# Performance work log

Hardware: AMD Instinct MI355X
Metric: run time of the kernel (lower is better)

Reference implementation:

```python
import jax, jax.numpy as jnp
import numpy as np
import math

EPS = 1e-5
GROUPS = 32

def group_norm(x, gamma, beta, groups=GROUPS, eps=EPS):
    B, C, H, W = x.shape
    xr = x.reshape(B, groups, C // groups, H, W)
    m = xr.mean(axis=(2, 3, 4), keepdims=True)
    v = xr.var(axis=(2, 3, 4), keepdims=True)
    xr = (xr - m) * jax.lax.rsqrt(v + eps)
    x = xr.reshape(B, C, H, W)
    return x * gamma[None, :, None, None] + beta[None, :, None, None]

def swish(x):
    return x * jax.nn.sigmoid(x)

def conv2d(x, w, b=None, padding='SAME'):
    # x: NCHW, w: OIHW
    y = jax.lax.conv_general_dilated(x, w, window_strides=(1, 1), padding=padding,
                                     dimension_numbers=('NCHW', 'OIHW', 'NCHW'))
    if b is not None:
        y = y + b[None, :, None, None]
    return y

def setup_inputs() -> dict:
    key = jax.random.key(0)
    ks = jax.random.split(key, 24)
    B, C, H, W = 16, 256, 32, 32
    NE = 256  # noise_level_emb_dim
    s = 0.02
    inp = {
        'x': jax.random.normal(ks[0], (B, C, H, W), jnp.float32),
        'time_emb': jax.random.normal(ks[1], (B, NE), jnp.float32),
        'c': jax.random.normal(ks[2], (B, C, H, W), jnp.float32),
        # block1: GroupNorm + Swish + Conv3x3(dim -> dim_out)
        'gn1_g': jnp.ones((C,), jnp.float32),
        'gn1_b': jnp.zeros((C,), jnp.float32),
        'conv1_w': jax.random.normal(ks[3], (C, C, 3, 3), jnp.float32) * s,
        'conv1_b': jnp.zeros((C,), jnp.float32),
        # FeatureWiseAffine linear (use_affine_level=False): Linear(NE -> dim_out)
        'noise_w': jax.random.normal(ks[4], (C, NE), jnp.float32) * s,
        'noise_b': jnp.zeros((C,), jnp.float32),
        # block2: GroupNorm + Swish + Conv3x3(dim_out -> dim_out)
        'gn2_g': jnp.ones((C,), jnp.float32),
        'gn2_b': jnp.zeros((C,), jnp.float32),
        'conv2_w': jax.random.normal(ks[5], (C, C, 3, 3), jnp.float32) * s,
        'conv2_b': jnp.zeros((C,), jnp.float32),
        # c_func: Conv1x1(dim_out -> dim_out)
        'cfunc_w': jax.random.normal(ks[6], (C, C, 1, 1), jnp.float32) * s,
        'cfunc_b': jnp.zeros((C,), jnp.float32),
        # attention: GroupNorm, qkv Conv1x1 (no bias), out Conv1x1
        'attn_gn_g': jnp.ones((C,), jnp.float32),
        'attn_gn_b': jnp.zeros((C,), jnp.float32),
        'qkv_w': jax.random.normal(ks[7], (3 * C, C, 1, 1), jnp.float32) * s,
        'out_w': jax.random.normal(ks[8], (C, C, 1, 1), jnp.float32) * s,
        'out_b': jnp.zeros((C,), jnp.float32),
    }
    return inp

def reference(x, time_emb, c,
              gn1_g, gn1_b, conv1_w, conv1_b,
              noise_w, noise_b,
              gn2_g, gn2_b, conv2_w, conv2_b,
              cfunc_w, cfunc_b,
              attn_gn_g, attn_gn_b, qkv_w, out_w, out_b):
    B, C, H, W = x.shape
    # ---- ResnetBlock ----
    h = conv2d(swish(group_norm(x, gn1_g, gn1_b)), conv1_w, conv1_b)
    # FeatureWiseAffine (additive): h + Linear(time_emb) broadcast over HxW
    h = h + (time_emb @ noise_w.T + noise_b)[:, :, None, None]
    h = conv2d(swish(group_norm(h, gn2_g, gn2_b)), conv2_w, conv2_b)
    h = conv2d(c, cfunc_w, cfunc_b) + h
    h = h + x  # res_conv is Identity since dim == dim_out
    # ---- SelfAttention (n_head=1) ----
    n = group_norm(h, attn_gn_g, attn_gn_b)
    qkv = conv2d(n, qkv_w)                       # [B, 3C, H, W]
    q, k, v = jnp.split(qkv.reshape(B, 3 * C, H * W), 3, axis=1)  # each [B, C, HW]
    scores = jnp.einsum('bcs,bct->bst', q, k) / math.sqrt(C)      # [B, HW, HW]
    attn = jax.nn.softmax(scores, axis=-1)
    o = jnp.einsum('bst,bct->bcs', attn, v).reshape(B, C, H, W)
    o = conv2d(o, out_w, out_b)
    return o + h
```

## Files before the change

kernel.cpp:

```cpp
#include <hip/hip_runtime.h>
#include <hip/hip_bf16.h>
#include <math.h>

typedef __hip_bfloat16 bf16;
typedef short short8 __attribute__((ext_vector_type(8)));
typedef float floatx4 __attribute__((ext_vector_type(4)));

#define NB 16
#define NC 256
#define NHW 1024
#define NNE 256
#define NP (NB*NC*NHW)

__device__ __forceinline__ unsigned short f2bu(float f){
  bf16 h = (bf16)f; return *(unsigned short*)&h;
}

__device__ __forceinline__ void gload_lds16(const short* g, short* l){
  __builtin_amdgcn_global_load_lds(
      (const __attribute__((address_space(1))) void*)g,
      (__attribute__((address_space(3))) void*)l, 16, 0, 0);
}

template<bool SWISH>
__global__ void gn_t_kernel(const float* __restrict__ src, const float* __restrict__ gamma,
                            const float* __restrict__ beta, short* __restrict__ xp){
  int b = blockIdx.x >> 5, g = blockIdx.x & 31;
  const int GSZ = 8*NHW;
  size_t base = ((size_t)b*NC + g*8)*NHW;
  int tid = threadIdx.x;
  float s = 0.f, ss = 0.f;
  for (int i = tid; i < GSZ; i += 256){
    float v = src[base+i];
    s += v; ss += v*v;
  }
  __shared__ float rs[256], rq[256];
  rs[tid] = s; rq[tid] = ss;
  __syncthreads();
  for (int off=128; off>0; off>>=1){
    if (tid < off){ rs[tid]+=rs[tid+off]; rq[tid]+=rq[tid+off]; }
    __syncthreads();
  }
  float mean = rs[0] * (1.f/GSZ);
  float var  = rq[0] * (1.f/GSZ) - mean*mean;
  float inv  = rsqrtf(var + 1e-5f);
  float gm[8], bt[8];
  #pragma unroll
  for (int j=0;j<8;j++){ gm[j] = gamma[g*8+j]*inv; bt[j] = beta[g*8+j]; }
  short* dst = xp + (((size_t)b*8 + (g>>2))*NHW)*32 + (g&3)*8;
  for (int px = tid; px < NHW; px += 256){
    short8 pk;
    #pragma unroll
    for (int j=0;j<8;j++){
      float v = (src[base + j*NHW + px] - mean)*gm[j] + bt[j];
      if (SWISH) v = v / (1.f + __expf(-v));
      pk[j] = (short)f2bu(v);
    }
    *(short8*)(dst + (size_t)px*32) = pk;
  }
}

template<bool SWISH>
__global__ void gn_post_kernel(const float* __restrict__ src, const float* __restrict__ st,
                               const float* __restrict__ gamma, const float* __restrict__ beta,
                               short* __restrict__ xp){
  int b = blockIdx.x >> 5, g = blockIdx.x & 31;
  size_t base = ((size_t)b*NC + g*8)*NHW;
  int tid = threadIdx.x;
  float s  = st[(b*32+g)*2+0];
  float ss = st[(b*32+g)*2+1];
  float mean = s * (1.f/8192.f);
  float var  = ss * (1.f/8192.f) - mean*mean;
  float inv  = rsqrtf(var + 1e-5f);
  float gm[8], bt[8];
  #pragma unroll
  for (int j=0;j<8;j++){ gm[j] = gamma[g*8+j]*inv; bt[j] = beta[g*8+j]; }
  short* dst = xp + (((size_t)b*8 + (g>>2))*NHW)*32 + (g&3)*8;
  for (int px = tid; px < NHW; px += 256){
    short8 pk;
    #pragma unroll
    for (int j=0;j<8;j++){
      float v = (src[base + j*NHW + px] - mean)*gm[j] + bt[j];
      if (SWISH) v = v / (1.f + __expf(-v));
      pk[j] = (short)f2bu(v);
    }
    *(short8*)(dst + (size_t)px*32) = pk;
  }
}

__global__ void wprep3_kernel(const float* __restrict__ w1, const float* __restrict__ w2,
                              short* __restrict__ wp1, short* __restrict__ wp2,
                              float* __restrict__ st){
  int co = blockIdx.x & 255;
  const float* w = (blockIdx.x < 256) ? w1 : w2;
  short* wp = (blockIdx.x < 256) ? wp1 : wp2;
  int tid = threadIdx.x;
  if (blockIdx.x == 0){
    for (int i=tid;i<4096;i+=256) st[i] = 0.f;
  }
  __shared__ float tmp[2304];
  for (int i=tid;i<2304;i+=256) tmp[i] = w[(size_t)co*2304 + i];
  __syncthreads();
  for (int j=tid;j<2304;j+=256){
    int tap = j>>8, ci = j&255;
    wp[(((size_t)tap*8 + (ci>>5))*NC + co)*32 + (ci&31)] = (short)f2bu(tmp[ci*9 + tap]);
  }
}

__global__ void wprep1_kernel(const float* __restrict__ wq, const float* __restrict__ wc,
                              const float* __restrict__ wo,
                              short* __restrict__ wqp, short* __restrict__ wcp,
                              short* __restrict__ wop){
  int blk = blockIdx.x, tid = threadIdx.x;
  if (blk < 768){
    float v = wq[(size_t)blk*256 + tid];
    wqp[(((size_t)(tid>>5))*768 + blk)*32 + (tid&31)] = (short)f2bu(v);
  } else if (blk < 1024){
    int co = blk - 768;
    float v = wc[(size_t)co*256 + tid];
    wcp[(((size_t)(tid>>5))*256 + co)*32 + (tid&31)] = (short)f2bu(v);
  } else {
    int co = blk - 1024;
    float v = wo[(size_t)co*256 + tid];
    wop[(((size_t)(tid>>5))*256 + co)*32 + (tid&31)] = (short)f2bu(v);
  }
}

__global__ void cvtc_kernel(const float* __restrict__ c_in, short* __restrict__ cp){
  int pxc = blockIdx.x, cc = blockIdx.y, b = blockIdx.z, tid = threadIdx.x;
  __shared__ float ld[32][257];
  size_t gbase = ((size_t)b*NC + cc*32)*NHW + pxc*256;
  for (int j=0;j<32;j++) ld[j][tid] = c_in[gbase + (size_t)j*NHW + tid];
  __syncthreads();
  short* dst = cp + (((size_t)b*8 + cc)*NHW + pxc*256)*32;
  for (int it=0;it<4;it++){
    int pxl = it*64 + (tid>>2), ckl = tid&3;
    short8 pk;
    #pragma unroll
    for (int e=0;e<8;e++) pk[e] = (short)f2bu(ld[ckl*8+e][pxl]);
    *(short8*)(dst + (size_t)pxl*32 + ckl*8) = pk;
  }
}

__global__ void noise_kernel(const float* __restrict__ emb, const float* __restrict__ w,
                             const float* __restrict__ bias, float* __restrict__ na){
  int b = blockIdx.x, c = threadIdx.x;
  __shared__ float e[NNE];
  e[c] = emb[b*NNE + c];
  __syncthreads();
  float acc = bias[c];
  for (int k=0;k<NNE;k++) acc += e[k]*w[c*NNE+k];
  na[b*NC + c] = acc;
}

__global__ __launch_bounds__(256,2)
void conv3_mfma_kernel(const short* __restrict__ xp, const short* __restrict__ wp,
                       const float* __restrict__ bias, const float* __restrict__ bias_bc,
                       const float* __restrict__ addf, float* __restrict__ out,
                       float* __restrict__ st, const short* __restrict__ zpad){
  const int b = blockIdx.z, bx = blockIdx.x, by = blockIdx.y;
  const int tid = threadIdx.x, wave = tid>>6, lane = tid&63;
  const int quad = lane>>4, lm = lane&15;
  const int co0 = by*64;
  const int px0 = bx*128, yb = bx*4;

  __shared__ short Sb0[12288], Sb1[12288], Sb2[12288];

  const int rowt = tid>>3;
  const int g2   = (tid&7) ^ ((tid>>3)&7);
  const int kq2  = g2 & 3;
  const int ccs2 = g2 >> 2;
  const size_t b8 = (size_t)b*8*NHW*32;

  auto STAGE = [&](int j, short* S){
    const int tap = j>>2, ccp = j&3;
    const int dyp = (tap*11)>>5;
    const int dx  = tap - dyp*3 - 1;
    const int dy  = dyp - 1;
    const short* wsrc = wp + (size_t)(tap*8 + ccp*2 + ccs2)*8192 + (co0 + rowt)*32 + kq2*8;
    #pragma unroll
    for (int i=0;i<2;i++)
      gload_lds16(wsrc + i*(32*32), S + tid*8 + i*2048);
    const short* xstep = xp + b8 + (size_t)(ccp*2 + ccs2)*(NHW*32);
    const int xx = rowt + dx;
    const bool xok = (unsigned)xx < 32u;
    #pragma unroll
    for (int i=0;i<4;i++){
      const int y = yb + i + dy;
      const short* src = (xok && (unsigned)y < 32u)
                       ? (xstep + (y*32 + xx)*32 + kq2*8)
                       : (zpad + kq2*8);
      gload_lds16(src, S + 4096 + tid*8 + i*2048);
    }
  };

  floatx4 acc[4][2];
  #pragma unroll
  for (int mt=0;mt<4;mt++)
    #pragma unroll
    for (int nt=0;nt<2;nt++) acc[mt][nt] = (floatx4){0.f,0.f,0.f,0.f};

  const int sl = lm & 7;
  auto STEP = [&](int j, short* S){
    asm volatile("s_waitcnt vmcnt(12)" ::: "memory");
    __builtin_amdgcn_s_barrier();
    __builtin_amdgcn_sched_barrier(0);
    short8 Af[2][4], Bf[2][2];
    #pragma unroll
    for (int ka=0;ka<2;ka++){
      const int slot = ((ka*4 + quad) ^ sl) << 3;
      #pragma unroll
      for (int mt=0;mt<4;mt++)
        Af[ka][mt] = *(const short8*)(S + (mt*16+lm)*64 + slot);
      #pragma unroll
      for (int nt=0;nt<2;nt++)
        Bf[ka][nt] = *(const short8*)(S + 4096 + (wave*32 + nt*16 + lm)*64 + slot);
    }
    asm volatile("s_waitcnt lgkmcnt(0)" ::: "memory");
    __builtin_amdgcn_sched_barrier(0);
    __builtin_amdgcn_s_barrier();
    int jn = j + 3; if (jn > 35) jn = 35;
    STAGE(jn, S);
    __builtin_amdgcn_s_setprio(1);
    #pragma unroll
    for (int ka=0;ka<2;ka++)
      #pragma unroll
      for (int mt=0;mt<4;mt++)
        #pragma unroll
        for (int nt=0;nt<2;nt++)
          acc[mt][nt] = __builtin_amdgcn_mfma_f32_16x16x32_bf16(Af[ka][mt], Bf[ka][nt], acc[mt][nt], 0,0,0);
    __builtin_amdgcn_s_setprio(0);
  };

  STAGE(0, Sb0); STAGE(1, Sb1); STAGE(2, Sb2);
  for (int jt=0; jt<36; jt+=3){
    STEP(jt+0, Sb0);
    STEP(jt+1, Sb1);
    STEP(jt+2, Sb2);
  }

  float gs[4], gq[4];
  #pragma unroll
  for (int mt=0;mt<4;mt++){ gs[mt]=0.f; gq[mt]=0.f; }
  #pragma unroll
  for (int mt=0;mt<4;mt++){
    #pragma unroll
    for (int r=0;r<4;r++){
      int co = co0 + mt*16 + quad*4 + r;
      float bb = bias[co] + (bias_bc ? bias_bc[b*NC + co] : 0.f);
      size_t ob = ((size_t)b*NC + co)*NHW + px0 + wave*32;
      #pragma unroll
      for (int nt=0;nt<2;nt++){
        size_t oi = ob + nt*16 + lm;
        float v = acc[mt][nt][r] + bb;
        if (addf) v += addf[oi];
        out[oi] = v;
        gs[mt] += v; gq[mt] += v*v;
      }
    }
  }
  #pragma unroll
  for (int mt=0;mt<4;mt++){
    float s = gs[mt], q = gq[mt];
    #pragma unroll
    for (int o=1;o<32;o<<=1){ s += __shfl_xor(s, o, 64); q += __shfl_xor(q, o, 64); }
    if ((lane&31) == 0){
      int g = (co0>>3) + mt*2 + (quad>>1);
      atomicAdd(&st[(b*32+g)*2+0], s);
      atomicAdd(&st[(b*32+g)*2+1], q);
    }
  }
}

__global__ __launch_bounds__(256)
void gemm_cfunc_kernel(const short* __restrict__ cp, const short* __restrict__ wcp,
                       const float* __restrict__ bias, const float* __restrict__ xres,
                       float* __restrict__ out){
  const int b = blockIdx.z;
  const int tid = threadIdx.x, wave = tid>>6, lane = tid&63;
  const int quad = lane>>4, lm = lane&15;
  const int M0 = blockIdx.y*128 + (wave>>1)*64;
  const int N0 = blockIdx.x*128 + (wave&1)*64;
  floatx4 acc[4][4];
  #pragma unroll
  for (int mt=0;mt<4;mt++)
    #pragma unroll
    for (int nt=0;nt<4;nt++) acc[mt][nt] = (floatx4){0.f,0.f,0.f,0.f};
  #pragma unroll
  for (int kk=0;kk<8;kk++){
    short8 af[4], bfr[4];
    #pragma unroll
    for (int mt=0;mt<4;mt++)
      af[mt] = *(const short8*)(wcp + ((size_t)kk*256 + M0 + mt*16 + lm)*32 + quad*8);
    #pragma unroll
    for (int nt=0;nt<4;nt++)
      bfr[nt] = *(const short8*)(cp + (((size_t)b*8 + kk)*NHW + N0 + nt*16 + lm)*32 + quad*8);
    #pragma unroll
    for (int mt=0;mt<4;mt++)
      #pragma unroll
      for (int nt=0;nt<4;nt++)
        acc[mt][nt] = __builtin_amdgcn_mfma_f32_16x16x32_bf16(af[mt], bfr[nt], acc[mt][nt], 0,0,0);
  }
  #pragma unroll
  for (int mt=0;mt<4;mt++){
    #pragma unroll
    for (int r=0;r<4;r++){
      int co = M0 + mt*16 + quad*4 + r;
      float bb = bias[co];
      size_t ob = ((size_t)b*NC + co)*NHW + N0;
      #pragma unroll
      for (int nt=0;nt<4;nt++){
        size_t oi = ob + nt*16 + lm;
        out[oi] = acc[mt][nt][r] + bb + xres[oi];
      }
    }
  }
}

__global__ __launch_bounds__(256)
void gemm_qkv_kernel(const short* __restrict__ ntp, const short* __restrict__ wqp,
                     short* __restrict__ qp, short* __restrict__ kp, short* __restrict__ vp){
  const int b = blockIdx.z;
  const int tid = threadIdx.x, wave = tid>>6, lane = tid&63;
  const int quad = lane>>4, lm = lane&15;
  const int M0 = blockIdx.y*128 + (wave>>1)*64;
  const int N0 = blockIdx.x*128 + (wave&1)*64;
  floatx4 acc[4][4];
  #pragma unroll
  for (int mt=0;mt<4;mt++)
    #pragma unroll
    for (int nt=0;nt<4;nt++) acc[mt][nt] = (floatx4){0.f,0.f,0.f,0.f};
  #pragma unroll
  for (int kk=0;kk<8;kk++){
    short8 af[4], bfr[4];
    #pragma unroll
    for (int mt=0;mt<4;mt++)
      af[mt] = *(const short8*)(wqp + ((size_t)kk*768 + M0 + mt*16 + lm)*32 + quad*8);
    #pragma unroll
    for (int nt=0;nt<4;nt++)
      bfr[nt] = *(const short8*)(ntp + (((size_t)b*8 + kk)*NHW + N0 + nt*16 + lm)*32 + quad*8);
    #pragma unroll
    for (int mt=0;mt<4;mt++)
      #pragma unroll
      for (int nt=0;nt<4;nt++)
        acc[mt][nt] = __builtin_amdgcn_mfma_f32_16x16x32_bf16(af[mt], bfr[nt], acc[mt][nt], 0,0,0);
  }
  #pragma unroll
  for (int mt=0;mt<4;mt++){
    int co_base = M0 + mt*16 + quad*4;
    int sec = co_base >> 8;
    int c = co_base & 255;
    #pragma unroll
    for (int nt=0;nt<4;nt++){
      int s = N0 + nt*16 + lm;
      if (sec < 2){
        unsigned short t0 = f2bu(acc[mt][nt][0]), t1 = f2bu(acc[mt][nt][1]);
        unsigned short t2 = f2bu(acc[mt][nt][2]), t3 = f2bu(acc[mt][nt][3]);
        uint2 w2; w2.x = ((unsigned)t1<<16)|t0; w2.y = ((unsigned)t3<<16)|t2;
        short* dst = (sec==0) ? qp : kp;
        *(uint2*)(dst + (((size_t)b*8 + (c>>5))*NHW + s)*32 + (c&31)) = w2;
      } else {
        #pragma unroll
        for (int r=0;r<4;r++)
          vp[(((size_t)b*32 + (s>>5))*NC + c + r)*32 + (s&31)] = (short)f2bu(acc[mt][nt][r]);
      }
    }
  }
}

__global__ __launch_bounds__(1024)
void attn_mfma_kernel(const short* __restrict__ qp, const short* __restrict__ kp,
                      const short* __restrict__ vp, short* __restrict__ op){
  const int bx = blockIdx.x;
  const int b = bx & 15;
  const int s0 = (bx >> 4) * 64;
  const int tid = threadIdx.x, wave = tid>>6, lane = tid&63;
  const int quad = lane>>4, lm = lane&15;

  __shared__ short P[64*1024];
  __shared__ float red[64][16];
  __shared__ float fred[64];

  floatx4 sc[4][4];
  #pragma unroll
  for (int rt=0;rt<4;rt++)
    #pragma unroll
    for (int ti=0;ti<4;ti++) sc[rt][ti] = (floatx4){0.f,0.f,0.f,0.f};

  const int colb = wave*64;
  #pragma unroll
  for (int h=0;h<8;h++){
    const size_t hb = ((size_t)b*8 + h)*NHW;
    short8 aq[4], kf[4];
    #pragma unroll
    for (int rt=0;rt<4;rt++)
      aq[rt] = *(const short8*)(qp + (hb + s0 + rt*16 + lm)*32 + quad*8);
    #pragma unroll
    for (int ti=0;ti<4;ti++)
      kf[ti] = *(const short8*)(kp + (hb + colb + ti*16 + lm)*32 + quad*8);
    #pragma unroll
    for (int rt=0;rt<4;rt++)
      #pragma unroll
      for (int ti=0;ti<4;ti++)
        sc[rt][ti] = __builtin_amdgcn_mfma_f32_16x16x32_bf16(aq[rt], kf[ti], sc[rt][ti], 0,0,0);
  }

  const float scale = 0.0625f;
  float mx[4][4];
  #pragma unroll
  for (int rt=0;rt<4;rt++)
    #pragma unroll
    for (int r=0;r<4;r++) mx[rt][r] = -1e30f;
  #pragma unroll
  for (int rt=0;rt<4;rt++)
    #pragma unroll
    for (int ti=0;ti<4;ti++)
      #pragma unroll
      for (int r=0;r<4;r++){
        float v = sc[rt][ti][r]*scale;
        sc[rt][ti][r] = v;
        mx[rt][r] = fmaxf(mx[rt][r], v);
      }
  #pragma unroll
  for (int o=1;o<16;o<<=1)
    #pragma unroll
    for (int rt=0;rt<4;rt++)
      #pragma unroll
      for (int r=0;r<4;r++) mx[rt][r] = fmaxf(mx[rt][r], __shfl_xor(mx[rt][r], o, 64));
  if (lm==0){
    #pragma unroll
    for (int rt=0;rt<4;rt++)
      #pragma unroll
      for (int r=0;r<4;r++) red[rt*16 + quad*4 + r][wave] = mx[rt][r];
  }
  __syncthreads();
  {
    float v = red[tid>>4][tid&15];
    #pragma unroll
    for (int o=1;o<16;o<<=1) v = fmaxf(v, __shfl_xor(v, o, 64));
    if ((tid&15)==0) fred[tid>>4] = v;
  }
  __syncthreads();
  float fmr[4][4], sm[4][4];
  #pragma unroll
  for (int rt=0;rt<4;rt++)
    #pragma unroll
    for (int r=0;r<4;r++){ fmr[rt][r] = fred[rt*16 + quad*4 + r]; sm[rt][r] = 0.f; }
  #pragma unroll
  for (int rt=0;rt<4;rt++)
    #pragma unroll
    for (int ti=0;ti<4;ti++)
      #pragma unroll
      for (int r=0;r<4;r++){
        float e = __expf(sc[rt][ti][r] - fmr[rt][r]);
        sc[rt][ti][r] = e;
        sm[rt][r] += e;
      }
  #pragma unroll
  for (int o=1;o<16;o<<=1)
    #pragma unroll
    for (int rt=0;rt<4;rt++)
      #pragma unroll
      for (int r=0;r<4;r++) sm[rt][r] += __shfl_xor(sm[rt][r], o, 64);
  __syncthreads();
  if (lm==0){
    #pragma unroll
    for (int rt=0;rt<4;rt++)
      #pragma unroll
      for (int r=0;r<4;r++) red[rt*16 + quad*4 + r][wave] = sm[rt][r];
  }
  __syncthreads();
  {
    float v = red[tid>>4][tid&15];
    #pragma unroll
    for (int o=1;o<16;o<<=1) v += __shfl_xor(v, o, 64);
    if ((tid&15)==0) fred[tid>>4] = 1.f/v;
  }
  __syncthreads();
  float fir[4][4];
  #pragma unroll
  for (int rt=0;rt<4;rt++)
    #pragma unroll
    for (int r=0;r<4;r++) fir[rt][r] = fred[rt*16 + quad*4 + r];
  #pragma unroll
  for (int rt=0;rt<4;rt++)
    #pragma unroll
    for (int ti=0;ti<4;ti++)
      #pragma unroll
      for (int r=0;r<4;r++){
        int row = rt*16 + quad*4 + r;
        int col = colb + ti*16 + lm;
        int off = row*1024 + ((((col>>3) ^ (row&7))&127)<<3) + (col&7);
        P[off] = (short)f2bu(sc[rt][ti][r]*fir[rt][r]);
      }
  __syncthreads();

  const int cg = wave>>1, sh = wave&1;
  const int ch0 = cg*32;
  floatx4 oacc[2][2];
  #pragma unroll
  for (int mt=0;mt<2;mt++)
    #pragma unroll
    for (int nt=0;nt<2;nt++) oacc[mt][nt] = (floatx4){0.f,0.f,0.f,0.f};

  #pragma unroll
  for (int kk=0;kk<32;kk++){
    short8 pf[2], vf[2];
    #pragma unroll
    for (int mt=0;mt<2;mt++){
      int row = sh*32 + mt*16 + lm;
      int off = row*1024 + ((((kk*4 + quad) ^ (row&7))&127)<<3);
      pf[mt] = *(const short8*)(&P[off]);
    }
    #pragma unroll
    for (int nt=0;nt<2;nt++)
      vf[nt] = *(const short8*)(vp + (((size_t)b*32 + kk)*NC + ch0 + nt*16 + lm)*32 + quad*8);
    #pragma unroll
    for (int mt=0;mt<2;mt++)
      #pragma unroll
      for (int nt=0;nt<2;nt++)
        oacc[mt][nt] = __builtin_amdgcn_mfma_f32_16x16x32_bf16(pf[mt], vf[nt], oacc[mt][nt], 0,0,0);
  }

  #pragma unroll
  for (int nt=0;nt<2;nt++){
    int c = ch0 + nt*16 + lm;
    int cc = c>>5, cl = c&31;
    #pragma unroll
    for (int mt=0;mt<2;mt++)
      #pragma unroll
      for (int r=0;r<4;r++){
        int s = s0 + sh*32 + mt*16 + quad*4 + r;
        op[(((size_t)b*8 + cc)*NHW + s)*32 + cl] = (short)f2bu(oacc[mt][nt][r]);
      }
  }
}

__global__ __launch_bounds__(256)
void outproj_mfma_kernel(const short* __restrict__ op, const short* __restrict__ wop,
                         const float* __restrict__ obias, const float* __restrict__ h,
                         float* __restrict__ out){
  const int b = blockIdx.z;
  const int tid = threadIdx.x, wave = tid>>6, lane = tid&63;
  const int quad = lane>>4, lm = lane&15;
  const int M0 = blockIdx.y*128 + (wave>>1)*64;
  const int N0 = blockIdx.x*128 + (wave&1)*64;
  floatx4 acc[4][4];
  #pragma unroll
  for (int mt=0;mt<4;mt++)
    #pragma unroll
    for (int nt=0;nt<4;nt++) acc[mt][nt] = (floatx4){0.f,0.f,0.f,0.f};
  #pragma unroll
  for (int kk=0;kk<8;kk++){
    short8 af[4], bfr[4];
    #pragma unroll
    for (int mt=0;mt<4;mt++)
      af[mt] = *(const short8*)(wop + ((size_t)kk*256 + M0 + mt*16 + lm)*32 + quad*8);
    #pragma unroll
    for (int nt=0;nt<4;nt++)
      bfr[nt] = *(const short8*)(op + (((size_t)b*8 + kk)*NHW + N0 + nt*16 + lm)*32 + quad*8);
    #pragma unroll
    for (int mt=0;mt<4;mt++)
      #pragma unroll
      for (int nt=0;nt<4;nt++)
        acc[mt][nt] = __builtin_amdgcn_mfma_f32_16x16x32_bf16(af[mt], bfr[nt], acc[mt][nt], 0,0,0);
  }
  #pragma unroll
  for (int mt=0;mt<4;mt++){
    #pragma unroll
    for (int r=0;r<4;r++){
      int co = M0 + mt*16 + quad*4 + r;
      float bb = obias[co];
      size_t ob = ((size_t)b*NC + co)*NHW + N0;
      #pragma unroll
      for (int nt=0;nt<4;nt++){
        size_t oi = ob + nt*16 + lm;
        out[oi] = acc[mt][nt][r] + bb + h[oi];
      }
    }
  }
}

extern "C" void kernel_launch(void* const* d_in, const int* in_sizes, int n_in,
                              void* d_out, int out_size, void* d_ws, size_t ws_size,
                              hipStream_t stream){
  const float* x        = (const float*)d_in[0];
  const float* time_emb = (const float*)d_in[1];
  const float* c_in     = (const float*)d_in[2];
  const float* gn1_g    = (const float*)d_in[3];
  const float* gn1_b    = (const float*)d_in[4];
  const float* conv1_w  = (const float*)d_in[5];
  const float* conv1_b  = (const float*)d_in[6];
  const float* noise_w  = (const float*)d_in[7];
  const float* noise_b  = (const float*)d_in[8];
  const float* gn2_g    = (const float*)d_in[9];
  const float* gn2_b    = (const float*)d_in[10];
  const float* conv2_w  = (const float*)d_in[11];
  const float* conv2_b  = (const float*)d_in[12];
  const float* cfunc_w  = (const float*)d_in[13];
  const float* cfunc_b  = (const float*)d_in[14];
  const float* agn_g    = (const float*)d_in[15];
  const float* agn_b    = (const float*)d_in[16];
  const float* qkv_w    = (const float*)d_in[17];
  const float* out_w    = (const float*)d_in[18];
  const float* out_b    = (const float*)d_in[19];
  float* outp = (float*)d_out;

  float* ws = (float*)d_ws;
  float* buf_h = ws;
  float* buf_t = buf_h + NP;
  short* xpb   = (short*)(buf_t + NP);
  short* qp    = xpb + NP;
  short* kp    = qp + NP;
  short* vp    = kp + NP;
  short* wp1   = vp + NP;
  short* wp2   = wp1 + 589824;
  short* wqp   = wp2 + 589824;
  short* wcp   = wqp + 196608;
  short* wop   = wcp + 65536;
  float* na    = (float*)(wop + 65536);
  float* st    = na + NB*NC;
  float* st2   = st;
  float* st3   = st + 1024;
  const short* zpadp = (const short*)(st + 2048);
  short* cp    = (short*)buf_t;
  short* op    = (short*)buf_t;

  wprep3_kernel<<<512, 256, 0, stream>>>(conv1_w, conv2_w, wp1, wp2, st);
  wprep1_kernel<<<1280, 256, 0, stream>>>(qkv_w, cfunc_w, out_w, wqp, wcp, wop);
  cvtc_kernel<<<dim3(4,8,NB), 256, 0, stream>>>(c_in, cp);
  noise_kernel<<<NB, 256, 0, stream>>>(time_emb, noise_w, noise_b, na);
  gn_t_kernel<true><<<NB*32, 256, 0, stream>>>(x, gn1_g, gn1_b, xpb);
  conv3_mfma_kernel<<<dim3(8, 4, NB), 256, 0, stream>>>(xpb, wp1, conv1_b, na, nullptr, buf_h, st2, zpadp);
  gn_post_kernel<true><<<NB*32, 256, 0, stream>>>(buf_h, st2, gn2_g, gn2_b, xpb);
  gemm_cfunc_kernel<<<dim3(8,2,NB), 256, 0, stream>>>(cp, wcp, cfunc_b, x, buf_h);
  conv3_mfma_kernel<<<dim3(8, 4, NB), 256, 0, stream>>>(xpb, wp2, conv2_b, nullptr, buf_h, buf_h, st3, zpadp);
  gn_post_kernel<false><<<NB*32, 256, 0, stream>>>(buf_h, st3, agn_g, agn_b, xpb);
  gemm_qkv_kernel<<<dim3(8,6,NB), 256, 0, stream>>>(xpb, wqp, qp, kp, vp);
  attn_mfma_kernel<<<256, 1024, 0, stream>>>(qp, kp, vp, op);
  outproj_mfma_kernel<<<dim3(8,2,NB), 256, 0, stream>>>(op, wop, out_b, buf_h, outp);
}
```

Baseline: 350.1 us.

## Load conv B-operand fragments directly into registers instead of staging through LDS

```diff
diff --git a/kernel.cpp b/kernel.cpp
--- a/kernel.cpp
+++ b/kernel.cpp
@@ -162,9 +162,10 @@
   const int tid = threadIdx.x, wave = tid>>6, lane = tid&63;
   const int quad = lane>>4, lm = lane&15;
   const int co0 = by*64;
-  const int px0 = bx*128, yb = bx*4;
-
-  __shared__ short Sb0[12288], Sb1[12288], Sb2[12288];
+  const int px0 = bx*128;
+  const int py  = bx*4 + wave;
+
+  __shared__ short Sb0[4096], Sb1[4096], Sb2[4096];
 
   const int rowt = tid>>3;
   const int g2   = (tid&7) ^ ((tid>>3)&7);
@@ -172,25 +173,29 @@
   const int ccs2 = g2 >> 2;
   const size_t b8 = (size_t)b*8*NHW*32;
 
-  auto STAGE = [&](int j, short* S){
+  auto STAGE_A = [&](int j, short* S){
+    const int tap = j>>2, ccp = j&3;
+    const short* wsrc = wp + (size_t)(tap*8 + ccp*2 + ccs2)*8192 + (co0 + rowt)*32 + kq2*8;
+    gload_lds16(wsrc,          S + tid*8);
+    gload_lds16(wsrc + 32*32,  S + tid*8 + 2048);
+  };
+
+  auto LOAD_B = [&](int j, short8* Br){
     const int tap = j>>2, ccp = j&3;
     const int dyp = (tap*11)>>5;
     const int dx  = tap - dyp*3 - 1;
-    const int dy  = dyp - 1;
-    const short* wsrc = wp + (size_t)(tap*8 + ccp*2 + ccs2)*8192 + (co0 + rowt)*32 + kq2*8;
-    #pragma unroll
-    for (int i=0;i<2;i++)
-      gload_lds16(wsrc + i*(32*32), S + tid*8 + i*2048);
-    const short* xstep = xp + b8 + (size_t)(ccp*2 + ccs2)*(NHW*32);
-    const int xx = rowt + dx;
-    const bool xok = (unsigned)xx < 32u;
-    #pragma unroll
-    for (int i=0;i<4;i++){
-      const int y = yb + i + dy;
-      const short* src = (xok && (unsigned)y < 32u)
-                       ? (xstep + (y*32 + xx)*32 + kq2*8)
-                       : (zpad + kq2*8);
-      gload_lds16(src, S + 4096 + tid*8 + i*2048);
+    const int sy  = py + dyp - 1;
+    const bool yok = (unsigned)sy < 32u;
+    #pragma unroll
+    for (int nt=0;nt<2;nt++){
+      const int xc = nt*16 + lm + dx;
+      const bool ok = yok && ((unsigned)xc < 32u);
+      #pragma unroll
+      for (int ka=0;ka<2;ka++){
+        const short* src = ok ? (xp + b8 + (size_t)(ccp*2+ka)*(NHW*32) + (sy*32+xc)*32 + quad*8)
+                              : (zpad + quad*8);
+        Br[ka*2+nt] = *(const short8*)src;
+      }
     }
   };
 
@@ -201,26 +206,23 @@
     for (int nt=0;nt<2;nt++) acc[mt][nt] = (floatx4){0.f,0.f,0.f,0.f};
 
   const int sl = lm & 7;
-  auto STEP = [&](int j, short* S){
-    asm volatile("s_waitcnt vmcnt(12)" ::: "memory");
+  auto STEP = [&](int j, short* S, short8* Br){
+    asm volatile("s_waitcnt vmcnt(4)" ::: "memory");
     __builtin_amdgcn_s_barrier();
     __builtin_amdgcn_sched_barrier(0);
-    short8 Af[2][4], Bf[2][2];
+    short8 Af[2][4];
     #pragma unroll
     for (int ka=0;ka<2;ka++){
       const int slot = ((ka*4 + quad) ^ sl) << 3;
       #pragma unroll
       for (int mt=0;mt<4;mt++)
         Af[ka][mt] = *(const short8*)(S + (mt*16+lm)*64 + slot);
-      #pragma unroll
-      for (int nt=0;nt<2;nt++)
-        Bf[ka][nt] = *(const short8*)(S + 4096 + (wave*32 + nt*16 + lm)*64 + slot);
     }
     asm volatile("s_waitcnt lgkmcnt(0)" ::: "memory");
     __builtin_amdgcn_sched_barrier(0);
     __builtin_amdgcn_s_barrier();
-    int jn = j + 3; if (jn > 35) jn = 35;
-    STAGE(jn, S);
+    int ja = j + 3; if (ja > 35) ja = 35;
+    STAGE_A(ja, S);
     __builtin_amdgcn_s_setprio(1);
     #pragma unroll
     for (int ka=0;ka<2;ka++)
@@ -228,17 +230,25 @@
       for (int mt=0;mt<4;mt++)
         #pragma unroll
         for (int nt=0;nt<2;nt++)
-          acc[mt][nt] = __builtin_amdgcn_mfma_f32_16x16x32_bf16(Af[ka][mt], Bf[ka][nt], acc[mt][nt], 0,0,0);
+          acc[mt][nt] = __builtin_amdgcn_mfma_f32_16x16x32_bf16(Af[ka][mt], Br[ka*2+nt], acc[mt][nt], 0,0,0);
     __builtin_amdgcn_s_setprio(0);
+    int jb = j + 2; if (jb > 35) jb = 35;
+    LOAD_B(jb, Br);
   };
 
-  STAGE(0, Sb0); STAGE(1, Sb1); STAGE(2, Sb2);
-  for (int jt=0; jt<36; jt+=3){
-    STEP(jt+0, Sb0);
-    STEP(jt+1, Sb1);
-    STEP(jt+2, Sb2);
-  }
-
+  short8 BrA[4], BrB[4];
+  STAGE_A(0, Sb0); STAGE_A(1, Sb1); STAGE_A(2, Sb2);
+  LOAD_B(0, BrA); LOAD_B(1, BrB);
+  for (int jt=0; jt<36; jt+=6){
+    STEP(jt+0, Sb0, BrA);
+    STEP(jt+1, Sb1, BrB);
+    STEP(jt+2, Sb2, BrA);
+    STEP(jt+3, Sb0, BrB);
+    STEP(jt+4, Sb1, BrA);
+    STEP(jt+5, Sb2, BrB);
+  }
+
+  const int hw0 = px0 + wave*32;
   float gs[4], gq[4];
   #pragma unroll
   for (int mt=0;mt<4;mt++){ gs[mt]=0.f; gq[mt]=0.f; }
@@ -248,7 +258,7 @@
     for (int r=0;r<4;r++){
       int co = co0 + mt*16 + quad*4 + r;
       float bb = bias[co] + (bias_bc ? bias_bc[b*NC + co] : 0.f);
-      size_t ob = ((size_t)b*NC + co)*NHW + px0 + wave*32;
+      size_t ob = ((size_t)b*NC + co)*NHW + hw0;
       #pragma unroll
       for (int nt=0;nt<2;nt++){
         size_t oi = ob + nt*16 + lm;
```

Measured after the change: 355.8 us. Within noise of the previous version (+1.6%).
